# Kernel tuning notes

Measured on AMD Instinct MI355X. Metric: run time of the kernel, lower is better.

Reference implementation:

```python
import jax, jax.numpy as jnp
import numpy as np

B, S, E, DK = 8, 2048, 1024, 64


def setup_inputs() -> dict:
    key = jax.random.key(0)
    ks = jax.random.split(key, 10)
    inv_e = 1.0 / np.sqrt(E)
    return {
        "k": jax.random.normal(ks[0], (B, S, E), dtype=jnp.float32),
        "q": jax.random.normal(ks[1], (B, S, E), dtype=jnp.float32),
        "v": jax.random.normal(ks[2], (B, S, E), dtype=jnp.float32),
        "mask": jax.random.randint(ks[3], (B, S, S), 0, 2, dtype=jnp.int32),
        "w_q": jax.random.uniform(ks[4], (DK, E), jnp.float32, -inv_e, inv_e),
        "b_q": jax.random.uniform(ks[5], (DK,), jnp.float32, -inv_e, inv_e),
        "w_k": jax.random.uniform(ks[6], (DK, E), jnp.float32, -inv_e, inv_e),
        "b_k": jax.random.uniform(ks[7], (DK,), jnp.float32, -inv_e, inv_e),
        "w_v": jax.random.uniform(ks[8], (DK, E), jnp.float32, -inv_e, inv_e),
        "b_v": jax.random.uniform(ks[9], (DK,), jnp.float32, -inv_e, inv_e),
    }


def reference(k, q, v, mask, w_q, b_q, w_k, b_k, w_v, b_v):
    # Linear projections: x @ W^T + b  -> [B, S, DK]
    K = jnp.einsum('bse,de->bsd', k, w_k) + b_k
    Q = jnp.einsum('bse,de->bsd', q, w_q) + b_q
    V = jnp.einsum('bse,de->bsd', v, w_v) + b_v
    scale = 1.0 / jnp.sqrt(jnp.asarray(DK, dtype=Q.dtype))
    scores = jnp.einsum('bqd,bkd->bqk', Q, K) * scale  # [B, S, S]
    scores = jnp.where(mask == 0, jnp.asarray(-1e9, scores.dtype), scores)
    attention_weights = jax.nn.softmax(scores, axis=2)
    attention_scores = jnp.einsum('bqk,bkd->bqd', attention_weights, V)
    return attention_scores, attention_weights
```

## Files before the change

### kernel.cpp

```cpp
#include <hip/hip_runtime.h>
#include <math.h>
#include <stdint.h>

#define BB 8
#define SS 2048
#define EE 1024
#define DKK 64

typedef _Float16 half8 __attribute__((ext_vector_type(8)));
typedef float floatx4 __attribute__((ext_vector_type(4)));

__device__ __forceinline__ void split8(float4 a, float4 b, half8& hi, half8& lo) {
  float va[8] = {a.x, a.y, a.z, a.w, b.x, b.y, b.z, b.w};
#pragma unroll
  for (int j = 0; j < 8; ++j) {
    _Float16 h = (_Float16)va[j];
    hi[j] = h;
    lo[j] = (_Float16)(va[j] - (float)h);
  }
}

__global__ __launch_bounds__(256, 3) void proj_kernel(
    const float* __restrict__ q_in, const float* __restrict__ k_in,
    const float* __restrict__ v_in,
    const float* __restrict__ w_q, const float* __restrict__ b_q,
    const float* __restrict__ w_k, const float* __restrict__ b_k,
    const float* __restrict__ w_v, const float* __restrict__ b_v,
    _Float16* __restrict__ Qh, _Float16* __restrict__ Kh,
    _Float16* __restrict__ VhT) {
  const int which = blockIdx.y;
  const float* X = which == 0 ? q_in : (which == 1 ? k_in : v_in);
  const float* W = which == 0 ? w_q : (which == 1 ? w_k : w_v);
  const float* bias = which == 0 ? b_q : (which == 1 ? b_k : b_v);

  __shared__ __align__(16) char Xh[64 * 128];
  __shared__ __align__(16) char Xl[64 * 128];
  __shared__ __align__(16) char Wh[64 * 128];
  __shared__ __align__(16) char Wl[64 * 128];

  const int t = threadIdx.x;
  const int row0 = blockIdx.x * 64;
  const int sr = t >> 2;
  const int c4 = t & 3;
  const int l = t & 63;
  const int li = l & 15, g = l >> 4;
  const int w = t >> 6;

  const float* xbase = X + (size_t)(row0 + sr) * EE + c4 * 16;
  const float* wbase = W + (size_t)sr * EE + c4 * 16;

  float4 xr[4], wr[4];
#pragma unroll
  for (int u = 0; u < 4; ++u) {
    xr[u] = ((const float4*)xbase)[u];
    wr[u] = ((const float4*)wbase)[u];
  }

  floatx4 acc[4];
#pragma unroll
  for (int c = 0; c < 4; ++c) acc[c] = (floatx4){0.f, 0.f, 0.f, 0.f};

  const int xrow_off = (w * 16 + li) * 128;
  const int swz = li & 7;

  for (int e0 = 0; e0 < EE; e0 += 64) {
    half8 xh0, xl0, xh1, xl1, wh0, wl0, wh1, wl1;
    split8(xr[0], xr[1], xh0, xl0);
    split8(xr[2], xr[3], xh1, xl1);
    split8(wr[0], wr[1], wh0, wl0);
    split8(wr[2], wr[3], wh1, wl1);
    __syncthreads();
    {
      const int p0 = ((c4 * 2 + 0) ^ (sr & 7)) * 16;
      const int p1 = ((c4 * 2 + 1) ^ (sr & 7)) * 16;
      *(half8*)(Xh + sr * 128 + p0) = xh0;
      *(half8*)(Xh + sr * 128 + p1) = xh1;
      *(half8*)(Xl + sr * 128 + p0) = xl0;
      *(half8*)(Xl + sr * 128 + p1) = xl1;
      *(half8*)(Wh + sr * 128 + p0) = wh0;
      *(half8*)(Wh + sr * 128 + p1) = wh1;
      *(half8*)(Wl + sr * 128 + p0) = wl0;
      *(half8*)(Wl + sr * 128 + p1) = wl1;
    }
    if (e0 + 64 < EE) {
#pragma unroll
      for (int u = 0; u < 4; ++u) {
        xr[u] = ((const float4*)(xbase + e0 + 64))[u];
        wr[u] = ((const float4*)(wbase + e0 + 64))[u];
      }
    }
    __syncthreads();
    half8 axh[2], axl[2];
#pragma unroll
    for (int h = 0; h < 2; ++h) {
      const int apos = ((h * 4 + g) ^ swz) * 16;
      axh[h] = *(const half8*)(Xh + xrow_off + apos);
      axl[h] = *(const half8*)(Xl + xrow_off + apos);
    }
#pragma unroll
    for (int c = 0; c < 4; ++c) {
      const int brow_off = (c * 16 + li) * 128;
#pragma unroll
      for (int h = 0; h < 2; ++h) {
        const int bpos = ((h * 4 + g) ^ swz) * 16;
        half8 bh = *(const half8*)(Wh + brow_off + bpos);
        half8 bl = *(const half8*)(Wl + brow_off + bpos);
        acc[c] = __builtin_amdgcn_mfma_f32_16x16x32_f16(axh[h], bh, acc[c], 0, 0, 0);
        acc[c] = __builtin_amdgcn_mfma_f32_16x16x32_f16(axh[h], bl, acc[c], 0, 0, 0);
        acc[c] = __builtin_amdgcn_mfma_f32_16x16x32_f16(axl[h], bh, acc[c], 0, 0, 0);
      }
    }
  }

  float bvv[4];
#pragma unroll
  for (int c = 0; c < 4; ++c) bvv[c] = bias[c * 16 + li];

  if (which < 2) {
    _Float16* P = (which == 0) ? Qh : Kh;
#pragma unroll
    for (int c = 0; c < 4; ++c)
#pragma unroll
      for (int r = 0; r < 4; ++r)
        P[(size_t)(row0 + w * 16 + g * 4 + r) * DKK + c * 16 + li] =
            (_Float16)(acc[c][r] + bvv[c]);
  } else {
    const int bb = row0 >> 11;
    const int s0 = row0 & (SS - 1);
#pragma unroll
    for (int c = 0; c < 4; ++c)
#pragma unroll
      for (int r = 0; r < 4; ++r)
        VhT[((size_t)bb * DKK + c * 16 + li) * SS + s0 + w * 16 + g * 4 + r] =
            (_Float16)(acc[c][r] + bvv[c]);
  }
}

__global__ __launch_bounds__(512, 4) void flash_kernel(
    const _Float16* __restrict__ Qh, const _Float16* __restrict__ Kh,
    const _Float16* __restrict__ VhT, const int* __restrict__ mask,
    float* __restrict__ outsc, uint32_t* __restrict__ mbits_g,
    float* __restrict__ mstats) {
  __shared__ __align__(16) char Vlds[16384];
  __shared__ uint32_t mwords[32][66];
  __shared__ float Obuf[32][68];
  __shared__ float mlbuf[8][16][2];
  __shared__ float lstat[32][2];

  const int t = threadIdx.x;
  const int b = (int)blockIdx.x & 7;
  const int q0 = ((int)blockIdx.x >> 3) * 32;
  const int l = t & 63;
  const int li = l & 15, g = l >> 4;
  const int w = t >> 6;
  const int qh = w & 1, ws = w >> 1;
  const float SCALE = 0.125f;

  {
    const int* mp = mask + ((size_t)b * SS + q0) * SS;
    uint32_t wbuf[4];
#pragma unroll
    for (int u = 0; u < 4; ++u) {
      const int word = t * 4 + u;
      const int4* src = (const int4*)(mp + word * 32);
      uint32_t bits = 0;
#pragma unroll
      for (int c = 0; c < 8; ++c) {
        int4 m4 = src[c];
        bits |= (uint32_t)(m4.x != 0) << (c * 4 + 0);
        bits |= (uint32_t)(m4.y != 0) << (c * 4 + 1);
        bits |= (uint32_t)(m4.z != 0) << (c * 4 + 2);
        bits |= (uint32_t)(m4.w != 0) << (c * 4 + 3);
      }
      wbuf[u] = bits;
      mwords[word >> 6][word & 63] = bits;
    }
    *(uint4*)(mbits_g + ((size_t)(b * SS + q0)) * 64 + t * 4) =
        *(const uint4*)wbuf;
  }

  half8 aq[2];
  {
    const _Float16* qp = Qh + ((size_t)b * SS + q0 + qh * 16 + li) * DKK;
    aq[0] = *(const half8*)(qp + g * 8);
    aq[1] = *(const half8*)(qp + 32 + g * 8);
  }

  float m_c = -3.0e38f, l_c = 0.f;
  floatx4 O[4];
#pragma unroll
  for (int d = 0; d < 4; ++d) O[d] = (floatx4){0.f, 0.f, 0.f, 0.f};

  half8 vv[2];
#pragma unroll
  for (int p = 0; p < 2; ++p) {
    const int slot = t + p * 512;
    const int vd = slot >> 4, vc = slot & 15;
    vv[p] = *(const half8*)(VhT + ((size_t)b * DKK + vd) * SS +
                            ((vc ^ (vd & 7)) * 8));
  }

  const _Float16* kbase = Kh + (size_t)b * SS * DKK;

  for (int kt = 0; kt < 16; ++kt) {
    __syncthreads();
#pragma unroll
    for (int p = 0; p < 2; ++p)
      *(half8*)(Vlds + (t + p * 512) * 16) = vv[p];
    __syncthreads();
    if (kt + 1 < 16) {
#pragma unroll
      for (int p = 0; p < 2; ++p) {
        const int slot = t + p * 512;
        const int vd = slot >> 4, vc = slot & 15;
        vv[p] = *(const half8*)(VhT + ((size_t)b * DKK + vd) * SS +
                                (kt + 1) * 128 + ((vc ^ (vd & 7)) * 8));
      }
    }

    half8 ka[2][2];
#pragma unroll
    for (int cb = 0; cb < 2; ++cb) {
      const int krow = ws * 32 + cb * 16 + li;
      const _Float16* kp = kbase + (size_t)(kt * 128 + krow) * DKK;
      ka[cb][0] = *(const half8*)(kp + g * 8);
      ka[cb][1] = *(const half8*)(kp + 32 + g * 8);
    }
    floatx4 sc[2];
#pragma unroll
    for (int cb = 0; cb < 2; ++cb) {
      floatx4 acc = {0.f, 0.f, 0.f, 0.f};
      acc = __builtin_amdgcn_mfma_f32_16x16x32_f16(ka[cb][0], aq[0], acc, 0, 0, 0);
      acc = __builtin_amdgcn_mfma_f32_16x16x32_f16(ka[cb][1], aq[1], acc, 0, 0, 0);
      sc[cb] = acc;
    }

    const uint32_t mw = mwords[qh * 16 + li][kt * 4 + ws];
    float p[2][4];
    float tmax = -3.0e38f;
#pragma unroll
    for (int cb = 0; cb < 2; ++cb)
#pragma unroll
      for (int r = 0; r < 4; ++r) {
        const float s =
            ((mw >> (cb * 16 + g * 4 + r)) & 1u) ? sc[cb][r] * SCALE : -1.0e9f;
        p[cb][r] = s;
        tmax = fmaxf(tmax, s);
      }
    tmax = fmaxf(tmax, __shfl_xor(tmax, 16));
    tmax = fmaxf(tmax, __shfl_xor(tmax, 32));
    const float m_new = fmaxf(m_c, tmax);
    const float alpha = __expf(m_c - m_new);
    m_c = m_new;
    float lsum = 0.f;
#pragma unroll
    for (int cb = 0; cb < 2; ++cb)
#pragma unroll
      for (int r = 0; r < 4; ++r) {
        p[cb][r] = __expf(p[cb][r] - m_new);
        lsum += p[cb][r];
      }
    l_c = l_c * alpha + lsum;

    half8 pB;
#pragma unroll
    for (int j = 0; j < 4; ++j) {
      pB[j] = (_Float16)p[0][j];
      pB[4 + j] = (_Float16)p[1][j];
    }

#pragma unroll
    for (int dblk = 0; dblk < 4; ++dblk) {
      const int d = dblk * 16 + li;
      const int rowb = d * 256;
      const int c1 = ws * 4 + (g >> 1);
      const int c2 = c1 + 2;
      const int sub = (g & 1) * 8;
      uint2 a1 = *(const uint2*)(Vlds + rowb + ((c1 ^ (li & 7)) * 16) + sub);
      uint2 a2 = *(const uint2*)(Vlds + rowb + ((c2 ^ (li & 7)) * 16) + sub);
      half8 av;
      *(uint2*)&av = a1;
      *((uint2*)&av + 1) = a2;
      O[dblk] = O[dblk] * alpha;
      O[dblk] = __builtin_amdgcn_mfma_f32_16x16x32_f16(av, pB, O[dblk], 0, 0, 0);
    }
  }

  l_c += __shfl_xor(l_c, 16);
  l_c += __shfl_xor(l_c, 32);
  if (g == 0) {
    mlbuf[w][li][0] = m_c;
    mlbuf[w][li][1] = l_c;
  }
  __syncthreads();
  float mstar = -3.0e38f;
#pragma unroll
  for (int p2 = 0; p2 < 4; ++p2)
    mstar = fmaxf(mstar, mlbuf[p2 * 2 + qh][li][0]);
  float lstar = 0.f;
#pragma unroll
  for (int p2 = 0; p2 < 4; ++p2)
    lstar += mlbuf[p2 * 2 + qh][li][1] * __expf(mlbuf[p2 * 2 + qh][li][0] - mstar);
  const float fown = __expf(m_c - mstar);
  if (g == 0 && ws == 0) {
    lstat[qh * 16 + li][0] = mstar;
    lstat[qh * 16 + li][1] = 1.f / lstar;
  }
#pragma unroll
  for (int dblk = 0; dblk < 4; ++dblk) O[dblk] = O[dblk] * fown;

  for (int ph = 0; ph < 4; ++ph) {
    if (ws == ph) {
      const int qq = qh * 16 + li;
#pragma unroll
      for (int dblk = 0; dblk < 4; ++dblk)
#pragma unroll
        for (int r = 0; r < 4; ++r) {
          const int d = dblk * 16 + g * 4 + r;
          if (ph == 0)
            Obuf[qq][d] = O[dblk][r];
          else
            Obuf[qq][d] += O[dblk][r];
        }
    }
    __syncthreads();
  }

  {
    const int qq = t >> 4;
    const int d0 = (t & 15) * 4;
    const float rl = lstat[qq][1];
    float4 o;
    o.x = Obuf[qq][d0 + 0] * rl;
    o.y = Obuf[qq][d0 + 1] * rl;
    o.z = Obuf[qq][d0 + 2] * rl;
    o.w = Obuf[qq][d0 + 3] * rl;
    *(float4*)(outsc + ((size_t)(b * SS + q0 + qq)) * DKK + d0) = o;
  }
  if (t < 32) {
    mstats[((size_t)(b * SS + q0 + t)) * 2 + 0] = lstat[t][0];
    mstats[((size_t)(b * SS + q0 + t)) * 2 + 1] = lstat[t][1];
  }
}

__global__ __launch_bounds__(512) void weights_kernel(
    const _Float16* __restrict__ Qh, const _Float16* __restrict__ Kh,
    const uint32_t* __restrict__ mbits_g, const float* __restrict__ mstats,
    float* __restrict__ wts) {
  const int t = threadIdx.x;
  const int b = (int)blockIdx.x & 7;
  const int q0 = ((int)blockIdx.x >> 3) * 32;
  const int l = t & 63;
  const int li = l & 15, g = l >> 4;
  const int w = t >> 6;
  const int qh = w & 1, cq = w >> 1;
  const float SCALE = 0.125f;

  half8 aq[2];
  {
    const _Float16* qp = Qh + ((size_t)b * SS + q0 + qh * 16 + li) * DKK;
    aq[0] = *(const half8*)(qp + g * 8);
    aq[1] = *(const half8*)(qp + 32 + g * 8);
  }
  float mr[4], rl[4];
#pragma unroll
  for (int r = 0; r < 4; ++r) {
    const size_t q = (size_t)b * SS + q0 + qh * 16 + g * 4 + r;
    mr[r] = mstats[q * 2 + 0];
    rl[r] = mstats[q * 2 + 1];
  }
  const _Float16* kbase = Kh + (size_t)b * SS * DKK;

  for (int kt = 0; kt < 16; ++kt) {
    uint32_t mw[4];
#pragma unroll
    for (int r = 0; r < 4; ++r)
      mw[r] = mbits_g[((size_t)(b * SS + q0 + qh * 16 + g * 4 + r)) * 64 +
                      kt * 4 + cq];
    half8 kb[2][2];
#pragma unroll
    for (int cb = 0; cb < 2; ++cb) {
      const int krow = cq * 32 + cb * 16 + li;
      const _Float16* kp = kbase + (size_t)(kt * 128 + krow) * DKK;
      kb[cb][0] = *(const half8*)(kp + g * 8);
      kb[cb][1] = *(const half8*)(kp + 32 + g * 8);
    }
#pragma unroll
    for (int cb = 0; cb < 2; ++cb) {
      floatx4 acc = {0.f, 0.f, 0.f, 0.f};
      acc = __builtin_amdgcn_mfma_f32_16x16x32_f16(aq[0], kb[cb][0], acc, 0, 0, 0);
      acc = __builtin_amdgcn_mfma_f32_16x16x32_f16(aq[1], kb[cb][1], acc, 0, 0, 0);
#pragma unroll
      for (int r = 0; r < 4; ++r) {
        const float wv = ((mw[r] >> (cb * 16 + li)) & 1u)
                             ? __expf(acc[r] * SCALE - mr[r]) * rl[r]
                             : 0.f;
        wts[((size_t)(b * SS + q0 + qh * 16 + g * 4 + r)) * SS + kt * 128 +
            cq * 32 + cb * 16 + li] = wv;
      }
    }
  }
}

extern "C" void kernel_launch(void* const* d_in, const int* in_sizes, int n_in,
                              void* d_out, int out_size, void* d_ws, size_t ws_size,
                              hipStream_t stream) {
  (void)in_sizes; (void)n_in; (void)out_size; (void)ws_size;
  const float* k_in = (const float*)d_in[0];
  const float* q_in = (const float*)d_in[1];
  const float* v_in = (const float*)d_in[2];
  const int* mask = (const int*)d_in[3];
  const float* w_q = (const float*)d_in[4];
  const float* b_q = (const float*)d_in[5];
  const float* w_k = (const float*)d_in[6];
  const float* b_k = (const float*)d_in[7];
  const float* w_v = (const float*)d_in[8];
  const float* b_v = (const float*)d_in[9];

  float* out_scores = (float*)d_out;
  float* out_weights = out_scores + (size_t)BB * SS * DKK;

  char* wsp = (char*)d_ws;
  const size_t nBSD = (size_t)BB * SS * DKK;
  _Float16* Qh = (_Float16*)wsp;
  _Float16* Kh = (_Float16*)(wsp + nBSD * 2);
  _Float16* VhT = (_Float16*)(wsp + nBSD * 4);
  uint32_t* mbits_g = (uint32_t*)(wsp + nBSD * 6);
  float* mstats = (float*)(wsp + nBSD * 6 + (size_t)BB * SS * 64 * 4);

  proj_kernel<<<dim3(256, 3), 256, 0, stream>>>(q_in, k_in, v_in, w_q, b_q,
                                                w_k, b_k, w_v, b_v, Qh, Kh, VhT);
  flash_kernel<<<512, 512, 0, stream>>>(Qh, Kh, VhT, mask, out_scores,
                                        mbits_g, mstats);
  weights_kernel<<<512, 512, 0, stream>>>(Qh, Kh, mbits_g, mstats, out_weights);
}
```

Measured before the change: 184.2 us.

## Pre-split weights to fp16 hi/lo once and load MFMA operands directly from global

Adds a small kernel that splits the three weight matrices into fp16 hi/lo halves once per call, instead of every projection block redoing that split. The projection kernel drops its LDS staging and both __syncthreads per step. Each lane now loads its X fragment straight from global memory with a one-step register prefetch, and reads the W hi/lo fragments directly from global/L2. This removes LDS traffic and barriers but adds an extra launch and uncoalesced-ish strided weight reads that depend on cache hits.

```diff
diff --git a/kernel.cpp b/kernel.cpp
--- a/kernel.cpp
+++ b/kernel.cpp
@@ -20,96 +20,69 @@
   }
 }
 
-__global__ __launch_bounds__(256, 3) void proj_kernel(
+__global__ __launch_bounds__(256) void wsplit_kernel(
+    const float* __restrict__ w_q, const float* __restrict__ w_k,
+    const float* __restrict__ w_v, _Float16* __restrict__ Whi,
+    _Float16* __restrict__ Wlo) {
+  const int idx = ((int)blockIdx.x * 256 + (int)threadIdx.x) * 8;
+  const int v = idx >> 16;
+  const int off = idx & 65535;
+  const float* W = v == 0 ? w_q : (v == 1 ? w_k : w_v);
+  float4 a = *(const float4*)(W + off);
+  float4 b = *(const float4*)(W + off + 4);
+  half8 hi, lo;
+  split8(a, b, hi, lo);
+  *(half8*)(Whi + idx) = hi;
+  *(half8*)(Wlo + idx) = lo;
+}
+
+__global__ __launch_bounds__(256) void proj_kernel(
     const float* __restrict__ q_in, const float* __restrict__ k_in,
     const float* __restrict__ v_in,
-    const float* __restrict__ w_q, const float* __restrict__ b_q,
-    const float* __restrict__ w_k, const float* __restrict__ b_k,
-    const float* __restrict__ w_v, const float* __restrict__ b_v,
+    const _Float16* __restrict__ Whi, const _Float16* __restrict__ Wlo,
+    const float* __restrict__ b_q, const float* __restrict__ b_k,
+    const float* __restrict__ b_v,
     _Float16* __restrict__ Qh, _Float16* __restrict__ Kh,
     _Float16* __restrict__ VhT) {
   const int which = blockIdx.y;
   const float* X = which == 0 ? q_in : (which == 1 ? k_in : v_in);
-  const float* W = which == 0 ? w_q : (which == 1 ? w_k : w_v);
   const float* bias = which == 0 ? b_q : (which == 1 ? b_k : b_v);
-
-  __shared__ __align__(16) char Xh[64 * 128];
-  __shared__ __align__(16) char Xl[64 * 128];
-  __shared__ __align__(16) char Wh[64 * 128];
-  __shared__ __align__(16) char Wl[64 * 128];
+  const _Float16* wh = Whi + which * 65536;
+  const _Float16* wl = Wlo + which * 65536;
 
   const int t = threadIdx.x;
-  const int row0 = blockIdx.x * 64;
-  const int sr = t >> 2;
-  const int c4 = t & 3;
   const int l = t & 63;
   const int li = l & 15, g = l >> 4;
   const int w = t >> 6;
-
-  const float* xbase = X + (size_t)(row0 + sr) * EE + c4 * 16;
-  const float* wbase = W + (size_t)sr * EE + c4 * 16;
-
-  float4 xr[4], wr[4];
-#pragma unroll
-  for (int u = 0; u < 4; ++u) {
-    xr[u] = ((const float4*)xbase)[u];
-    wr[u] = ((const float4*)wbase)[u];
-  }
+  const int row0 = (int)blockIdx.x * 64;
+  const float* xrow = X + (size_t)(row0 + w * 16 + li) * EE + g * 8;
 
   floatx4 acc[4];
 #pragma unroll
   for (int c = 0; c < 4; ++c) acc[c] = (floatx4){0.f, 0.f, 0.f, 0.f};
 
-  const int xrow_off = (w * 16 + li) * 128;
-  const int swz = li & 7;
-
-  for (int e0 = 0; e0 < EE; e0 += 64) {
-    half8 xh0, xl0, xh1, xl1, wh0, wl0, wh1, wl1;
-    split8(xr[0], xr[1], xh0, xl0);
-    split8(xr[2], xr[3], xh1, xl1);
-    split8(wr[0], wr[1], wh0, wl0);
-    split8(wr[2], wr[3], wh1, wl1);
-    __syncthreads();
-    {
-      const int p0 = ((c4 * 2 + 0) ^ (sr & 7)) * 16;
-      const int p1 = ((c4 * 2 + 1) ^ (sr & 7)) * 16;
-      *(half8*)(Xh + sr * 128 + p0) = xh0;
-      *(half8*)(Xh + sr * 128 + p1) = xh1;
-      *(half8*)(Xl + sr * 128 + p0) = xl0;
-      *(half8*)(Xl + sr * 128 + p1) = xl1;
-      *(half8*)(Wh + sr * 128 + p0) = wh0;
-      *(half8*)(Wh + sr * 128 + p1) = wh1;
-      *(half8*)(Wl + sr * 128 + p0) = wl0;
-      *(half8*)(Wl + sr * 128 + p1) = wl1;
-    }
-    if (e0 + 64 < EE) {
-#pragma unroll
-      for (int u = 0; u < 4; ++u) {
-        xr[u] = ((const float4*)(xbase + e0 + 64))[u];
-        wr[u] = ((const float4*)(wbase + e0 + 64))[u];
-      }
-    }
-    __syncthreads();
-    half8 axh[2], axl[2];
-#pragma unroll
-    for (int h = 0; h < 2; ++h) {
-      const int apos = ((h * 4 + g) ^ swz) * 16;
-      axh[h] = *(const half8*)(Xh + xrow_off + apos);
-      axl[h] = *(const half8*)(Xl + xrow_off + apos);
-    }
+  float4 xa = ((const float4*)xrow)[0];
+  float4 xb = ((const float4*)xrow)[1];
+  for (int e0 = 0; e0 < EE; e0 += 32) {
+    float4 na, nb;
+    if (e0 + 32 < EE) {
+      na = ((const float4*)(xrow + e0 + 32))[0];
+      nb = ((const float4*)(xrow + e0 + 32))[1];
+    }
+    half8 axh, axl;
+    split8(xa, xb, axh, axl);
+    const int wo = e0 + g * 8;
 #pragma unroll
     for (int c = 0; c < 4; ++c) {
-      const int brow_off = (c * 16 + li) * 128;
-#pragma unroll
-      for (int h = 0; h < 2; ++h) {
-        const int bpos = ((h * 4 + g) ^ swz) * 16;
-        half8 bh = *(const half8*)(Wh + brow_off + bpos);
-        half8 bl = *(const half8*)(Wl + brow_off + bpos);
-        acc[c] = __builtin_amdgcn_mfma_f32_16x16x32_f16(axh[h], bh, acc[c], 0, 0, 0);
-        acc[c] = __builtin_amdgcn_mfma_f32_16x16x32_f16(axh[h], bl, acc[c], 0, 0, 0);
-        acc[c] = __builtin_amdgcn_mfma_f32_16x16x32_f16(axl[h], bh, acc[c], 0, 0, 0);
-      }
-    }
+      const int wrow = (c * 16 + li) * EE + wo;
+      const half8 bh = *(const half8*)(wh + wrow);
+      const half8 bl = *(const half8*)(wl + wrow);
+      acc[c] = __builtin_amdgcn_mfma_f32_16x16x32_f16(axh, bh, acc[c], 0, 0, 0);
+      acc[c] = __builtin_amdgcn_mfma_f32_16x16x32_f16(axh, bl, acc[c], 0, 0, 0);
+      acc[c] = __builtin_amdgcn_mfma_f32_16x16x32_f16(axl, bh, acc[c], 0, 0, 0);
+    }
+    xa = na;
+    xb = nb;
   }
 
   float bvv[4];
@@ -427,9 +400,13 @@
   _Float16* VhT = (_Float16*)(wsp + nBSD * 4);
   uint32_t* mbits_g = (uint32_t*)(wsp + nBSD * 6);
   float* mstats = (float*)(wsp + nBSD * 6 + (size_t)BB * SS * 64 * 4);
-
-  proj_kernel<<<dim3(256, 3), 256, 0, stream>>>(q_in, k_in, v_in, w_q, b_q,
-                                                w_k, b_k, w_v, b_v, Qh, Kh, VhT);
+  _Float16* Whi = (_Float16*)(wsp + nBSD * 6 + (size_t)BB * SS * 64 * 4 +
+                              (size_t)BB * SS * 2 * 4);
+  _Float16* Wlo = Whi + 3 * 65536;
+
+  wsplit_kernel<<<96, 256, 0, stream>>>(w_q, w_k, w_v, Whi, Wlo);
+  proj_kernel<<<dim3(256, 3), 256, 0, stream>>>(q_in, k_in, v_in, Whi, Wlo,
+                                                b_q, b_k, b_v, Qh, Kh, VhT);
   flash_kernel<<<512, 512, 0, stream>>>(Qh, Kh, VhT, mask, out_scores,
                                         mbits_g, mstats);
   weights_kernel<<<512, 512, 0, stream>>>(Qh, Kh, mbits_g, mstats, out_weights);
```

New measurement: 250.2 us. +35.8%, slower.
